# Performance work log

Measured on AMD Instinct MI355X. Metric: run time of the kernel, lower is better.

Reference implementation:

```python
import jax, jax.numpy as jnp
import numpy as np

MODEL_DIM = 1024
NUM_HEADS = 16
K_DIM = MODEL_DIM // NUM_HEADS


def setup_inputs() -> dict:
    key = jax.random.key(0)
    kx, kw1, kw2 = jax.random.split(key, 3)
    B, L, D = 4, 2048, MODEL_DIM
    x = jax.random.normal(kx, (B, L, D), dtype=jnp.float32)
    # nn.Linear(D, 3D, bias=False): y = x @ W^T; store transposed form [D, 3D]
    scale1 = 1.0 / np.sqrt(D)
    Wqkv = jax.random.uniform(kw1, (D, 3 * D), dtype=jnp.float32, minval=-scale1, maxval=scale1)
    Wout = jax.random.uniform(kw2, (D, D), dtype=jnp.float32, minval=-scale1, maxval=scale1)
    return {"x": x, "Wqkv": Wqkv, "Wout": Wout}


def reference(x, Wqkv, Wout):
    B, L, D = x.shape
    H, Kd = NUM_HEADS, K_DIM
    qkv = x @ Wqkv  # [B, L, 3D]
    q, k, v = jnp.split(qkv, 3, axis=-1)

    def heads(t):  # [B, L, D] -> [B, H, L, Kd]
        return t.reshape(B, L, H, Kd).transpose(0, 2, 1, 3)

    qh, kh, vh = heads(q), heads(k), heads(v)
    scores = jnp.einsum('bhqd,bhkd->bhqk', qh, kh) / jnp.sqrt(jnp.float32(Kd))
    causal = jnp.triu(jnp.ones((L, L), dtype=bool), k=1)  # True above diagonal
    scores = jnp.where(causal, -jnp.inf, scores)
    probs = jax.nn.softmax(scores, axis=-1)
    attended = jnp.einsum('bhqk,bhkd->bhqd', probs, vh)
    concatted = attended.transpose(0, 2, 1, 3).reshape(B, L, D)
    # dropout is identity in eval mode
    return concatted @ Wout
```

## Files before the change

kernel.cpp:

```cpp
#include <hip/hip_runtime.h>

typedef unsigned short u16;
typedef unsigned int   u32;
typedef __bf16   bf16x8 __attribute__((ext_vector_type(8)));
typedef float    f32x4  __attribute__((ext_vector_type(4)));
typedef u16      u16x4  __attribute__((ext_vector_type(4)));
typedef u16      u16x8  __attribute__((ext_vector_type(8)));
typedef u32      u32x2  __attribute__((ext_vector_type(2)));
typedef u32      u32x4  __attribute__((ext_vector_type(4)));

#if __has_builtin(__builtin_amdgcn_exp2f)
#define EXP2(x) __builtin_amdgcn_exp2f(x)
#else
#define EXP2(x) exp2f(x)
#endif

__device__ __forceinline__ u16 f2bf(float f) {
    unsigned u = __float_as_uint(f);
    u += 0x7FFFu + ((u >> 16) & 1u);
    return (u16)(u >> 16);
}

__device__ __forceinline__ u32 pack_bf16(float a, float b) {
#if __has_builtin(__builtin_amdgcn_cvt_pk_bf16_f32)
    typedef __bf16 bf16x2 __attribute__((ext_vector_type(2)));
    bf16x2 r = __builtin_amdgcn_cvt_pk_bf16_f32(a, b);
    return __builtin_bit_cast(u32, r);
#else
    return (u32)f2bf(a) | ((u32)f2bf(b) << 16);
#endif
}

__device__ __forceinline__ void async_copy16(const u16* g, u16* l) {
    __builtin_amdgcn_global_load_lds(
        (const __attribute__((address_space(1))) unsigned*)g,
        (__attribute__((address_space(3))) unsigned*)l, 16, 0, 0);
}

__device__ __forceinline__ bf16x8 lds_frag(const u16* p) {
    return *(const bf16x8*)p;
}

__global__ __launch_bounds__(256) void prep(const float* __restrict__ x,
                                            const float* __restrict__ Wqkv,
                                            const float* __restrict__ Wout,
                                            u16* __restrict__ xb,
                                            u16* __restrict__ wqkv_t,
                                            u16* __restrict__ wout_t) {
    __shared__ u16 t[64 * 72];
    const int bid = blockIdx.x;
    const int tid = threadIdx.x;

    if (bid >= 1024) {
        size_t i = ((size_t)(bid - 1024) * 256 + tid) * 8;
        float4 v0 = *(const float4*)(x + i);
        float4 v1 = *(const float4*)(x + i + 4);
        u16x8 o = { f2bf(v0.x), f2bf(v0.y), f2bf(v0.z), f2bf(v0.w),
                    f2bf(v1.x), f2bf(v1.y), f2bf(v1.z), f2bf(v1.w) };
        *(u16x8*)(xb + i) = o;
        return;
    }

    const float* W;  u16* Wt;  int Kd, Nd, n0, k0;
    if (bid < 768) { W = Wqkv; Wt = wqkv_t; Kd = 1024; Nd = 3072;
                     n0 = (bid % 48) * 64; k0 = (bid / 48) * 64; }
    else           { W = Wout; Wt = wout_t; Kd = 1024; Nd = 1024;
                     n0 = ((bid - 768) % 16) * 64; k0 = ((bid - 768) / 16) * 64; }
#pragma unroll
    for (int i = 0; i < 4; ++i) {
        int lin = i * 256 + tid;
        int kr = lin >> 4, nc = (lin & 15) << 2;
        float4 v = *(const float4*)(W + (size_t)(k0 + kr) * Nd + n0 + nc);
        u16x4 o = { f2bf(v.x), f2bf(v.y), f2bf(v.z), f2bf(v.w) };
        *(u16x4*)&t[kr * 72 + nc] = o;
    }
    __syncthreads();
#pragma unroll
    for (int i = 0; i < 2; ++i) {
        int lin = i * 256 + tid;
        int nr = lin >> 3, kc = (lin & 7) << 3;
        u16x8 o;
#pragma unroll
        for (int jj = 0; jj < 8; ++jj) o[jj] = t[(kc + jj) * 72 + nr];
        *(u16x8*)(Wt + (size_t)(n0 + nr) * Kd + k0 + kc) = o;
    }
}

__global__ __launch_bounds__(256) void gemm_qkv(const u16* __restrict__ A,
                                                const u16* __restrict__ Bt,
                                                u16* __restrict__ outb,
                                                int K, int N) {
    __shared__ u16 As[2][128 * 32];
    __shared__ u16 Bs[2][128 * 32];
    const int tid = threadIdx.x;
    const int lane = tid & 63;
    const int wv = tid >> 6;
    const int wr = (wv >> 1) * 64;
    const int wc = (wv & 1) * 64;
    const int qd = lane >> 4;
    const int c  = lane & 15;
    const int m0 = blockIdx.y * 128;
    const int n0 = blockIdx.x * 128;

    const int srow = tid >> 2;
    const int sg = ((tid & 3) ^ ((srow >> 1) & 3)) << 3;

    const u16* Ag0 = A  + (size_t)(m0 +      srow) * K + sg;
    const u16* Ag1 = A  + (size_t)(m0 + 64 + srow) * K + sg;
    const u16* Bg0 = Bt + (size_t)(n0 +      srow) * K + sg;
    const u16* Bg1 = Bt + (size_t)(n0 + 64 + srow) * K + sg;

    const u32 fsw = (qd ^ ((c >> 1) & 3)) << 3;
    const u32 a_off = (wr + c) * 32 + fsw;
    const u32 b_off = (wc + c) * 32 + fsw;

    f32x4 acc[4][4] = {};

    async_copy16(Ag0, &As[0][tid * 8]);
    async_copy16(Ag1, &As[0][2048 + tid * 8]);
    async_copy16(Bg0, &Bs[0][tid * 8]);
    async_copy16(Bg1, &Bs[0][2048 + tid * 8]);

    int p = 0;
    for (int k0 = 0; k0 < K; k0 += 32) {
        __syncthreads();
        if (k0 + 32 < K) {
            const int np = p ^ 1;
            async_copy16(Ag0 + k0 + 32, &As[np][tid * 8]);
            async_copy16(Ag1 + k0 + 32, &As[np][2048 + tid * 8]);
            async_copy16(Bg0 + k0 + 32, &Bs[np][tid * 8]);
            async_copy16(Bg1 + k0 + 32, &Bs[np][2048 + tid * 8]);
        }
        bf16x8 af[4], bfr[4];
#pragma unroll
        for (int i = 0; i < 4; ++i) af[i]  = lds_frag(&As[p][a_off + i * 512]);
#pragma unroll
        for (int j = 0; j < 4; ++j) bfr[j] = lds_frag(&Bs[p][b_off + j * 512]);
#pragma unroll
        for (int i = 0; i < 4; ++i)
#pragma unroll
            for (int j = 0; j < 4; ++j)
                acc[i][j] = __builtin_amdgcn_mfma_f32_16x16x32_bf16(af[i], bfr[j], acc[i][j], 0, 0, 0);
        p ^= 1;
    }

#pragma unroll
    for (int i = 0; i < 4; ++i)
#pragma unroll
        for (int j = 0; j < 4; ++j) {
            int n = n0 + wc + j * 16 + c;
            int which = n >> 10, h = (n >> 6) & 15, kd = n & 63;
            int m_base = m0 + wr + i * 16 + qd * 4;
            int b = m_base >> 11, l0 = m_base & 2047;
            int bh = b * 16 + h;
            if (which == 2) {
                u32x2 o2;
                o2[0] = pack_bf16(acc[i][j][0], acc[i][j][1]);
                o2[1] = pack_bf16(acc[i][j][2], acc[i][j][3]);
                *(u32x2*)(outb + (size_t)(128 + bh) * 131072 + (size_t)kd * 2048 + l0) = o2;
            } else if (which == 0) {
#pragma unroll
                for (int r = 0; r < 4; ++r)
                    outb[(size_t)bh * 131072 + (size_t)(l0 + r) * 64 + kd] =
                        f2bf(acc[i][j][r] * 0.1803368801f);
            } else {
#pragma unroll
                for (int r = 0; r < 4; ++r)
                    outb[(size_t)(64 + bh) * 131072 + (size_t)(l0 + r) * 64 + kd] =
                        f2bf(acc[i][j][r]);
            }
        }
}

__global__ __launch_bounds__(256) void gemm_out(const u16* __restrict__ A,
                                                const u16* __restrict__ Bt,
                                                float* __restrict__ outf,
                                                int K, int N) {
    __shared__ u16 As[2][64 * 32];
    __shared__ u16 Bs[2][128 * 32];
    const int tid = threadIdx.x;
    const int lane = tid & 63;
    const int wv = tid >> 6;
    const int wr = (wv >> 1) * 32;
    const int wc = (wv & 1) * 64;
    const int qd = lane >> 4;
    const int c  = lane & 15;
    const int m0 = blockIdx.y * 64;
    const int n0 = blockIdx.x * 128;

    const int srow = tid >> 2;
    const int sg = ((tid & 3) ^ ((srow >> 1) & 3)) << 3;

    const u16* Ag0 = A  + (size_t)(m0 +      srow) * K + sg;
    const u16* Bg0 = Bt + (size_t)(n0 +      srow) * K + sg;
    const u16* Bg1 = Bt + (size_t)(n0 + 64 + srow) * K + sg;

    const u32 fsw = (qd ^ ((c >> 1) & 3)) << 3;
    const u32 a_off = (wr + c) * 32 + fsw;
    const u32 b_off = (wc + c) * 32 + fsw;

    f32x4 acc[2][4] = {};

    async_copy16(Ag0, &As[0][tid * 8]);
    async_copy16(Bg0, &Bs[0][tid * 8]);
    async_copy16(Bg1, &Bs[0][2048 + tid * 8]);

    int p = 0;
    for (int k0 = 0; k0 < K; k0 += 32) {
        __syncthreads();
        if (k0 + 32 < K) {
            const int np = p ^ 1;
            async_copy16(Ag0 + k0 + 32, &As[np][tid * 8]);
            async_copy16(Bg0 + k0 + 32, &Bs[np][tid * 8]);
            async_copy16(Bg1 + k0 + 32, &Bs[np][2048 + tid * 8]);
        }
        bf16x8 af[2], bfr[4];
#pragma unroll
        for (int i = 0; i < 2; ++i) af[i]  = lds_frag(&As[p][a_off + i * 512]);
#pragma unroll
        for (int j = 0; j < 4; ++j) bfr[j] = lds_frag(&Bs[p][b_off + j * 512]);
#pragma unroll
        for (int i = 0; i < 2; ++i)
#pragma unroll
            for (int j = 0; j < 4; ++j)
                acc[i][j] = __builtin_amdgcn_mfma_f32_16x16x32_bf16(af[i], bfr[j], acc[i][j], 0, 0, 0);
        p ^= 1;
    }

#pragma unroll
    for (int i = 0; i < 2; ++i)
#pragma unroll
        for (int j = 0; j < 4; ++j)
#pragma unroll
            for (int r = 0; r < 4; ++r) {
                int m = m0 + wr + i * 16 + qd * 4 + r;
                int n = n0 + wc + j * 16 + c;
                outf[(size_t)m * N + n] = acc[i][j][r];
            }
}

__global__ __launch_bounds__(256, 2) void attn_kernel(const u16* __restrict__ qkv,
                                                      u16* __restrict__ att) {
    __shared__ u16 Ks[2][128 * 64];
    __shared__ u16 Vt[2][64 * 128];
    __shared__ u16 Ps[4][16 * 128];

    const int tid = threadIdx.x;
    const int lane = tid & 63;
    const int w = tid >> 6;
    const int qd = lane >> 4;
    const int c = lane & 15;

    const int flat = blockIdx.x + 8 * blockIdx.y;
    const int bh = (flat & 7) + 8 * ((flat >> 3) & 7);
    const int bx = flat >> 6;
    const int b = bh >> 4, h = bh & 15;

    const u16* Qg = qkv + (size_t)bh * 131072;
    const u16* Kg = qkv + (size_t)(64 + bh) * 131072;
    const u16* Vg = qkv + (size_t)(128 + bh) * 131072;

    u32 k_go[4], v_go[4], s_lo[4];
#pragma unroll
    for (int it = 0; it < 4; ++it) {
        int lin = it * 256 + tid;
        int krw = lin >> 3, kch = lin & 7;
        k_go[it] = krw * 64 + ((kch ^ (krw & 7)) << 3);
        int vrw = lin >> 4, vch = lin & 15;
        v_go[it] = vrw * 2048 + ((vch ^ (vrw & 15)) << 3);
        s_lo[it] = lin * 8;
    }

    u32 kf_off[2];
#pragma unroll
    for (int ks = 0; ks < 2; ++ks)
        kf_off[ks] = c * 64 + (((ks * 4 + qd) ^ (c & 7)) << 3);
    u32 vf_off[4];
#pragma unroll
    for (int kc = 0; kc < 4; ++kc)
        vf_off[kc] = c * 128 + (((kc * 4 + qd) ^ c) << 3);
    u16* psw = &Ps[w][c * 128 + (qd & 1) * 4];
    const u16* psr = &Ps[w][c * 128];

#pragma unroll
    for (int seg = 0; seg < 2; ++seg) {
        const int qt = seg ? (15 - bx) : bx;
        const int qa_row = qt * 128 + w * 32 + c;
        const int qb_row = qa_row + 16;

        bf16x8 qa[2], qb[2];
#pragma unroll
        for (int ks = 0; ks < 2; ++ks) {
            qa[ks] = *(const bf16x8*)(Qg + (size_t)qa_row * 64 + ks * 32 + qd * 8);
            qb[ks] = *(const bf16x8*)(Qg + (size_t)qb_row * 64 + ks * 32 + qd * 8);
        }

        f32x4 acca[4] = {}, accb[4] = {};
        float ra = 0.0f, rb = 0.0f;

        const int nkt = qt + 1;
        int p = 0;
        for (int kt = 0; kt < nkt; ++kt) {
            __syncthreads();
            if (kt == 0) {
#pragma unroll
                for (int it = 0; it < 4; ++it) {
                    async_copy16(Kg + (size_t)kt * 8192 + k_go[it], &Ks[0][s_lo[it]]);
                    async_copy16(Vg + (size_t)kt * 128  + v_go[it], &Vt[0][s_lo[it]]);
                }
                __syncthreads();
            }
            if (kt + 1 < nkt) {
                const int nt = kt + 1, np = p ^ 1;
#pragma unroll
                for (int it = 0; it < 4; ++it) {
                    async_copy16(Kg + (size_t)nt * 8192 + k_go[it], &Ks[np][s_lo[it]]);
                    async_copy16(Vg + (size_t)nt * 128  + v_go[it], &Vt[np][s_lo[it]]);
                }
            }

            const u16* ksb = Ks[p];
            const u16* vtb = Vt[p];

            f32x4 sa[8] = {}, sb[8] = {};
#pragma unroll
            for (int ks = 0; ks < 2; ++ks) {
                const u16* kp = ksb + kf_off[ks];
#pragma unroll
                for (int f = 0; f < 8; ++f) {
                    bf16x8 kf = lds_frag(kp + f * 1024);
                    sa[f] = __builtin_amdgcn_mfma_f32_16x16x32_bf16(kf, qa[ks], sa[f], 0, 0, 0);
                    sb[f] = __builtin_amdgcn_mfma_f32_16x16x32_bf16(kf, qb[ks], sb[f], 0, 0, 0);
                }
            }

            if (kt == qt) {
#pragma unroll
                for (int f = 0; f < 8; ++f)
#pragma unroll
                    for (int r = 0; r < 4; ++r) {
                        int key = kt * 128 + f * 16 + qd * 4 + r;
                        if (key > qa_row) sa[f][r] = -3e38f;
                        if (key > qb_row) sb[f][r] = -3e38f;
                    }
            }

#pragma unroll
            for (int f = 0; f < 8; ++f)
#pragma unroll
                for (int r = 0; r < 4; ++r) {
                    float pa = EXP2(sa[f][r] - 8.0f);
                    float pb = EXP2(sb[f][r] - 8.0f);
                    sa[f][r] = pa; sb[f][r] = pb;
                    ra += pa; rb += pb;
                }

            u32x4 pfa[4], pfb[4];
#pragma unroll
            for (int f = 0; f < 8; ++f) {
                u32x2 pw;
                pw[0] = pack_bf16(sa[f][0], sa[f][1]);
                pw[1] = pack_bf16(sa[f][2], sa[f][3]);
                *(u32x2*)(psw + (((f * 2 + (qd >> 1)) ^ c) << 3)) = pw;
            }
#pragma unroll
            for (int kc = 0; kc < 4; ++kc)
                pfa[kc] = *(const u32x4*)(psr + (((kc * 4 + qd) ^ c) << 3));
#pragma unroll
            for (int f = 0; f < 8; ++f) {
                u32x2 pw;
                pw[0] = pack_bf16(sb[f][0], sb[f][1]);
                pw[1] = pack_bf16(sb[f][2], sb[f][3]);
                *(u32x2*)(psw + (((f * 2 + (qd >> 1)) ^ c) << 3)) = pw;
            }
#pragma unroll
            for (int kc = 0; kc < 4; ++kc)
                pfb[kc] = *(const u32x4*)(psr + (((kc * 4 + qd) ^ c) << 3));

#pragma unroll
            for (int kc = 0; kc < 4; ++kc) {
                const u16* vp = vtb + vf_off[kc];
                bf16x8 pa = __builtin_bit_cast(bf16x8, pfa[kc]);
                bf16x8 pb = __builtin_bit_cast(bf16x8, pfb[kc]);
#pragma unroll
                for (int jo = 0; jo < 4; ++jo) {
                    bf16x8 vf = lds_frag(vp + jo * 2048);
                    acca[jo] = __builtin_amdgcn_mfma_f32_16x16x32_bf16(vf, pa, acca[jo], 0, 0, 0);
                    accb[jo] = __builtin_amdgcn_mfma_f32_16x16x32_bf16(vf, pb, accb[jo], 0, 0, 0);
                }
            }
            p ^= 1;
        }

        ra += __shfl_xor(ra, 16, 64);
        ra += __shfl_xor(ra, 32, 64);
        rb += __shfl_xor(rb, 16, 64);
        rb += __shfl_xor(rb, 32, 64);
        float ia = __builtin_amdgcn_rcpf(ra), ib = __builtin_amdgcn_rcpf(rb);
        u16* ar = att + ((size_t)b * 2048 + qa_row) * 1024 + h * 64;
        u16* br = att + ((size_t)b * 2048 + qb_row) * 1024 + h * 64;
#pragma unroll
        for (int jo = 0; jo < 4; ++jo) {
            u32x2 oa, ob;
            oa[0] = pack_bf16(acca[jo][0] * ia, acca[jo][1] * ia);
            oa[1] = pack_bf16(acca[jo][2] * ia, acca[jo][3] * ia);
            ob[0] = pack_bf16(accb[jo][0] * ib, accb[jo][1] * ib);
            ob[1] = pack_bf16(accb[jo][2] * ib, accb[jo][3] * ib);
            *(u32x2*)(ar + jo * 16 + qd * 4) = oa;
            *(u32x2*)(br + jo * 16 + qd * 4) = ob;
        }
    }
}

extern "C" void kernel_launch(void* const* d_in, const int* in_sizes, int n_in,
                              void* d_out, int out_size, void* d_ws, size_t ws_size,
                              hipStream_t stream) {
    const float* x    = (const float*)d_in[0];
    const float* Wqkv = (const float*)d_in[1];
    const float* Wout = (const float*)d_in[2];
    float* out = (float*)d_out;

    char* ws = (char*)d_ws;
    u16* x_bf   = (u16*)(ws);
    u16* wqkv_t = (u16*)(ws + 16777216);
    u16* wout_t = (u16*)(ws + 23068672);
    u16* qkv_h  = (u16*)(ws + 25165824);
    u16* att    = (u16*)(ws + 75497472);

    prep<<<dim3(5120), dim3(256), 0, stream>>>(x, Wqkv, Wout, x_bf, wqkv_t, wout_t);
    gemm_qkv<<<dim3(24, 64), dim3(256), 0, stream>>>(x_bf, wqkv_t, qkv_h, 1024, 3072);
    attn_kernel<<<dim3(8, 64), dim3(256), 0, stream>>>(qkv_h, att);
    gemm_out<<<dim3(8, 128), dim3(256), 0, stream>>>(att, wout_t, out, 1024, 1024);
}
```

Measured before the change: 251.7 us.

## Software-pipeline QK^T with PV, swap P through permlanes instead of LDS

Restructures the attention inner loop so the S=QK^T MFMAs for the next key tile are issued before the softmax/PV of the current tile, using two S register sets and a triple-buffered V in LDS. The P-matrix transpose, which used to go through a per-wave LDS scratch buffer, now uses v_permlane32/16_swap register shuffles. The -8 bias is folded into the accumulator init, row sums are kept as vectors, and s_setprio is raised around the MFMA blocks. The goal is to overlap matrix and exp/pack work and cut LDS traffic. In exchange it uses more registers, which at 2 blocks per CU could cause spills or lower occupancy.

New measurement: 270.2 us. 1.07x slower.

```diff
diff --git a/kernel.cpp b/kernel.cpp
--- a/kernel.cpp
+++ b/kernel.cpp
@@ -39,6 +39,13 @@
 
 __device__ __forceinline__ bf16x8 lds_frag(const u16* p) {
     return *(const bf16x8*)p;
+}
+
+__device__ __forceinline__ void permlane32_swap(u32& a, u32& b) {
+    asm("v_permlane32_swap_b32 %0, %1" : "+v"(a), "+v"(b));
+}
+__device__ __forceinline__ void permlane16_swap(u32& a, u32& b) {
+    asm("v_permlane16_swap_b32 %0, %1" : "+v"(a), "+v"(b));
 }
 
 __global__ __launch_bounds__(256) void prep(const float* __restrict__ x,
@@ -242,8 +249,7 @@
 __global__ __launch_bounds__(256, 2) void attn_kernel(const u16* __restrict__ qkv,
                                                       u16* __restrict__ att) {
     __shared__ u16 Ks[2][128 * 64];
-    __shared__ u16 Vt[2][64 * 128];
-    __shared__ u16 Ps[4][16 * 128];
+    __shared__ u16 Vt[3][64 * 128];
 
     const int tid = threadIdx.x;
     const int lane = tid & 63;
@@ -260,17 +266,6 @@
     const u16* Kg = qkv + (size_t)(64 + bh) * 131072;
     const u16* Vg = qkv + (size_t)(128 + bh) * 131072;
 
-    u32 k_go[4], v_go[4], s_lo[4];
-#pragma unroll
-    for (int it = 0; it < 4; ++it) {
-        int lin = it * 256 + tid;
-        int krw = lin >> 3, kch = lin & 7;
-        k_go[it] = krw * 64 + ((kch ^ (krw & 7)) << 3);
-        int vrw = lin >> 4, vch = lin & 15;
-        v_go[it] = vrw * 2048 + ((vch ^ (vrw & 15)) << 3);
-        s_lo[it] = lin * 8;
-    }
-
     u32 kf_off[2];
 #pragma unroll
     for (int ks = 0; ks < 2; ++ks)
@@ -279,10 +274,21 @@
 #pragma unroll
     for (int kc = 0; kc < 4; ++kc)
         vf_off[kc] = c * 128 + (((kc * 4 + qd) ^ c) << 3);
-    u16* psw = &Ps[w][c * 128 + (qd & 1) * 4];
-    const u16* psr = &Ps[w][c * 128];
-
-#pragma unroll
+
+    auto issue_copy = [&](int t, u16* kd, u16* vd) {
+#pragma unroll
+        for (int it = 0; it < 4; ++it) {
+            int lin = it * 256 + tid;
+            int krw = lin >> 3, kch = lin & 7;
+            int vrw = lin >> 4, vch = lin & 15;
+            async_copy16(Kg + (size_t)t * 8192 + krw * 64 + ((kch ^ (krw & 7)) << 3),
+                         kd + lin * 8);
+            async_copy16(Vg + (size_t)t * 128 + (size_t)vrw * 2048 + ((vch ^ (vrw & 15)) << 3),
+                         vd + lin * 8);
+        }
+    };
+
+#pragma unroll 1
     for (int seg = 0; seg < 2; ++seg) {
         const int qt = seg ? (15 - bx) : bx;
         const int qa_row = qt * 128 + w * 32 + c;
@@ -296,33 +302,18 @@
         }
 
         f32x4 acca[4] = {}, accb[4] = {};
-        float ra = 0.0f, rb = 0.0f;
+        f32x4 rva = {}, rvb = {};
+        f32x4 saA[8], sbA[8], saB[8], sbB[8];
 
         const int nkt = qt + 1;
-        int p = 0;
-        for (int kt = 0; kt < nkt; ++kt) {
-            __syncthreads();
-            if (kt == 0) {
-#pragma unroll
-                for (int it = 0; it < 4; ++it) {
-                    async_copy16(Kg + (size_t)kt * 8192 + k_go[it], &Ks[0][s_lo[it]]);
-                    async_copy16(Vg + (size_t)kt * 128  + v_go[it], &Vt[0][s_lo[it]]);
-                }
-                __syncthreads();
-            }
-            if (kt + 1 < nkt) {
-                const int nt = kt + 1, np = p ^ 1;
-#pragma unroll
-                for (int it = 0; it < 4; ++it) {
-                    async_copy16(Kg + (size_t)nt * 8192 + k_go[it], &Ks[np][s_lo[it]]);
-                    async_copy16(Vg + (size_t)nt * 128  + v_go[it], &Vt[np][s_lo[it]]);
-                }
-            }
-
-            const u16* ksb = Ks[p];
-            const u16* vtb = Vt[p];
-
-            f32x4 sa[8] = {}, sb[8] = {};
+
+        auto compute_S = [&](const u16* ksb, f32x4* sa, f32x4* sb) {
+#pragma unroll
+            for (int f = 0; f < 8; ++f) {
+                sa[f] = f32x4{-8.f, -8.f, -8.f, -8.f};
+                sb[f] = f32x4{-8.f, -8.f, -8.f, -8.f};
+            }
+            __builtin_amdgcn_s_setprio(1);
 #pragma unroll
             for (int ks = 0; ks < 2; ++ks) {
                 const u16* kp = ksb + kf_off[ks];
@@ -333,7 +324,10 @@
                     sb[f] = __builtin_amdgcn_mfma_f32_16x16x32_bf16(kf, qb[ks], sb[f], 0, 0, 0);
                 }
             }
-
+            __builtin_amdgcn_s_setprio(0);
+        };
+
+        auto finish_tile = [&](int kt, f32x4* sa, f32x4* sb, const u16* vtb) {
             if (kt == qt) {
 #pragma unroll
                 for (int f = 0; f < 8; ++f)
@@ -344,54 +338,83 @@
                         if (key > qb_row) sb[f][r] = -3e38f;
                     }
             }
-
-#pragma unroll
-            for (int f = 0; f < 8; ++f)
+#pragma unroll
+            for (int f = 0; f < 8; ++f) {
 #pragma unroll
                 for (int r = 0; r < 4; ++r) {
-                    float pa = EXP2(sa[f][r] - 8.0f);
-                    float pb = EXP2(sb[f][r] - 8.0f);
-                    sa[f][r] = pa; sb[f][r] = pb;
-                    ra += pa; rb += pb;
+                    sa[f][r] = EXP2(sa[f][r]);
+                    sb[f][r] = EXP2(sb[f][r]);
                 }
-
-            u32x4 pfa[4], pfb[4];
-#pragma unroll
-            for (int f = 0; f < 8; ++f) {
-                u32x2 pw;
-                pw[0] = pack_bf16(sa[f][0], sa[f][1]);
-                pw[1] = pack_bf16(sa[f][2], sa[f][3]);
-                *(u32x2*)(psw + (((f * 2 + (qd >> 1)) ^ c) << 3)) = pw;
-            }
-#pragma unroll
-            for (int kc = 0; kc < 4; ++kc)
-                pfa[kc] = *(const u32x4*)(psr + (((kc * 4 + qd) ^ c) << 3));
-#pragma unroll
-            for (int f = 0; f < 8; ++f) {
-                u32x2 pw;
-                pw[0] = pack_bf16(sb[f][0], sb[f][1]);
-                pw[1] = pack_bf16(sb[f][2], sb[f][3]);
-                *(u32x2*)(psw + (((f * 2 + (qd >> 1)) ^ c) << 3)) = pw;
-            }
-#pragma unroll
-            for (int kc = 0; kc < 4; ++kc)
-                pfb[kc] = *(const u32x4*)(psr + (((kc * 4 + qd) ^ c) << 3));
-
+                rva += sa[f];
+                rvb += sb[f];
+            }
 #pragma unroll
             for (int kc = 0; kc < 4; ++kc) {
+                u32 a0 = pack_bf16(sa[2 * kc][0], sa[2 * kc][1]);
+                u32 a1 = pack_bf16(sa[2 * kc + 1][0], sa[2 * kc + 1][1]);
+                u32 b0 = pack_bf16(sa[2 * kc][2], sa[2 * kc][3]);
+                u32 b1 = pack_bf16(sa[2 * kc + 1][2], sa[2 * kc + 1][3]);
+                permlane32_swap(a0, a1); permlane16_swap(a0, a1);
+                permlane32_swap(b0, b1); permlane16_swap(b0, b1);
+                u32x4 wa = {a0, b0, a1, b1};
+                u32 c0 = pack_bf16(sb[2 * kc][0], sb[2 * kc][1]);
+                u32 c1 = pack_bf16(sb[2 * kc + 1][0], sb[2 * kc + 1][1]);
+                u32 d0 = pack_bf16(sb[2 * kc][2], sb[2 * kc][3]);
+                u32 d1 = pack_bf16(sb[2 * kc + 1][2], sb[2 * kc + 1][3]);
+                permlane32_swap(c0, c1); permlane16_swap(c0, c1);
+                permlane32_swap(d0, d1); permlane16_swap(d0, d1);
+                u32x4 wb = {c0, d0, c1, d1};
+                bf16x8 pa = __builtin_bit_cast(bf16x8, wa);
+                bf16x8 pb = __builtin_bit_cast(bf16x8, wb);
                 const u16* vp = vtb + vf_off[kc];
-                bf16x8 pa = __builtin_bit_cast(bf16x8, pfa[kc]);
-                bf16x8 pb = __builtin_bit_cast(bf16x8, pfb[kc]);
+                __builtin_amdgcn_s_setprio(1);
 #pragma unroll
                 for (int jo = 0; jo < 4; ++jo) {
                     bf16x8 vf = lds_frag(vp + jo * 2048);
                     acca[jo] = __builtin_amdgcn_mfma_f32_16x16x32_bf16(vf, pa, acca[jo], 0, 0, 0);
                     accb[jo] = __builtin_amdgcn_mfma_f32_16x16x32_bf16(vf, pb, accb[jo], 0, 0, 0);
                 }
-            }
-            p ^= 1;
-        }
-
+                __builtin_amdgcn_s_setprio(0);
+            }
+        };
+
+        __syncthreads();
+        issue_copy(0, Ks[0], Vt[0]);
+        __syncthreads();
+        if (nkt > 1) issue_copy(1, Ks[1], Vt[1]);
+        compute_S(Ks[0], saA, sbA);
+
+        u16 *vPV = Vt[0], *vNx = Vt[1], *vFr = Vt[2];
+
+        int kt = 0;
+        for (;;) {
+            {
+                const bool last = (kt + 1 >= nkt);
+                if (!last) {
+                    __syncthreads();
+                    if (kt + 2 < nkt) issue_copy(kt + 2, Ks[0], vFr);
+                    compute_S(Ks[1], saB, sbB);
+                }
+                finish_tile(kt, saA, sbA, vPV);
+                if (last) break;
+                u16* t0 = vPV; vPV = vNx; vNx = vFr; vFr = t0;
+            }
+            {
+                const bool last = (kt + 2 >= nkt);
+                if (!last) {
+                    __syncthreads();
+                    if (kt + 3 < nkt) issue_copy(kt + 3, Ks[1], vFr);
+                    compute_S(Ks[0], saA, sbA);
+                }
+                finish_tile(kt + 1, saB, sbB, vPV);
+                if (last) break;
+                u16* t0 = vPV; vPV = vNx; vNx = vFr; vFr = t0;
+            }
+            kt += 2;
+        }
+
+        float ra = rva[0] + rva[1] + rva[2] + rva[3];
+        float rb = rvb[0] + rvb[1] + rvb[2] + rvb[3];
         ra += __shfl_xor(ra, 16, 64);
         ra += __shfl_xor(ra, 32, 64);
         rb += __shfl_xor(rb, 16, 64);
```
